# Performance work log

Measured on AMD Instinct MI355X. Metric: run time of the kernel, lower is better.

Reference implementation:

```python
import jax, jax.numpy as jnp
import numpy as np

B, H, W, C, NH, WS, SS = 32, 56, 56, 192, 6, 7, 3
L = H * W
N = WS * WS
HD = C // NH
EPS = 1e-3  # keras LayerNormalization default epsilon


def _rel_index(ws):
    coords = np.stack(np.meshgrid(np.arange(ws), np.arange(ws), indexing='ij')).reshape(2, -1)
    rel = (coords[:, :, None] - coords[:, None, :]).transpose(1, 2, 0)
    rel[..., 0] += ws - 1
    rel[..., 1] += ws - 1
    rel[..., 0] *= 2 * ws - 1
    return rel.sum(-1)  # (N, N) int


def _attn_mask(h, w, ws, ss):
    img = np.zeros((h, w), np.float32)
    cnt = 0
    for hs in (slice(0, -ws), slice(-ws, -ss), slice(-ss, None)):
        for wsl in (slice(0, -ws), slice(-ws, -ss), slice(-ss, None)):
            img[hs, wsl] = cnt
            cnt += 1
    mw = img.reshape(h // ws, ws, w // ws, ws).transpose(0, 2, 1, 3).reshape(-1, ws * ws)
    diff = mw[:, None, :] - mw[:, :, None]  # expand_dims(mw,1) - expand_dims(mw,2)
    return np.where(diff != 0, -100.0, 0.0).astype(np.float32)  # (nW, N, N)


REL_IDX = _rel_index(WS)
ATTN_MASK = _attn_mask(H, W, WS, SS)


def _ln(x, g, b):
    m = x.mean(-1, keepdims=True)
    v = x.var(-1, keepdims=True)
    return (x - m) / jnp.sqrt(v + EPS) * g + b


def setup_inputs() -> dict:
    key = jax.random.key(0)
    ks = jax.random.split(key, 8)
    s = 0.02
    return {
        'x': jax.random.normal(ks[0], (B, L, C), jnp.float32),
        'gamma1': jnp.ones((C,), jnp.float32),
        'beta1': jnp.zeros((C,), jnp.float32),
        'qkv_w': jax.random.normal(ks[1], (C, 3 * C), jnp.float32) * s,
        'qkv_b': jnp.zeros((3 * C,), jnp.float32),
        'proj_w': jax.random.normal(ks[2], (C, C), jnp.float32) * s,
        'proj_b': jnp.zeros((C,), jnp.float32),
        'rel_bias_table': jax.random.normal(ks[3], ((2 * WS - 1) ** 2, NH), jnp.float32) * s,
        'gamma2': jnp.ones((C,), jnp.float32),
        'beta2': jnp.zeros((C,), jnp.float32),
        'fc1_w': jax.random.normal(ks[4], (C, 4 * C), jnp.float32) * s,
        'fc1_b': jnp.zeros((4 * C,), jnp.float32),
        'fc2_w': jax.random.normal(ks[5], (4 * C, C), jnp.float32) * s,
        'fc2_b': jnp.zeros((C,), jnp.float32),
    }


def reference(x, gamma1, beta1, qkv_w, qkv_b, proj_w, proj_b, rel_bias_table,
              gamma2, beta2, fc1_w, fc1_b, fc2_w, fc2_b):
    scale = HD ** -0.5
    shortcut = x
    # norm1 + cyclic shift + window partition
    xn = _ln(x, gamma1, beta1).reshape(B, H, W, C)
    xn = jnp.roll(xn, (-SS, -SS), axis=(1, 2))
    xw = xn.reshape(B, H // WS, WS, W // WS, WS, C).transpose(0, 1, 3, 2, 4, 5).reshape(-1, N, C)
    # window attention
    qkv = (xw @ qkv_w + qkv_b).reshape(-1, N, 3, NH, HD).transpose(2, 0, 3, 1, 4)
    q, k, v = qkv[0] * scale, qkv[1], qkv[2]  # (B*nW, NH, N, HD)
    attn = jnp.einsum('whnd,whmd->whnm', q, k)
    bias = rel_bias_table[REL_IDX.reshape(-1)].reshape(N, N, NH).transpose(2, 0, 1)
    attn = attn + bias[None]
    nW = ATTN_MASK.shape[0]
    attn = attn.reshape(B, nW, NH, N, N) + jnp.asarray(ATTN_MASK)[None, :, None]
    attn = jax.nn.softmax(attn.reshape(-1, NH, N, N), axis=-1)
    out = jnp.einsum('whnm,whmd->whnd', attn, v).transpose(0, 2, 1, 3).reshape(-1, N, C)
    out = out @ proj_w + proj_b
    # window reverse + reverse shift
    xr = out.reshape(B, H // WS, W // WS, WS, WS, C).transpose(0, 1, 3, 2, 4, 5).reshape(B, H, W, C)
    xr = jnp.roll(xr, (SS, SS), axis=(1, 2)).reshape(B, L, C)
    x = shortcut + xr
    # MLP block
    y = _ln(x, gamma2, beta2)
    y = jax.nn.gelu(y @ fc1_w + fc1_b, approximate=False) @ fc2_w + fc2_b
    return x + y
```

## Files before the change

### kernel.cpp

```cpp
#include <hip/hip_runtime.h>
#include <math.h>

namespace {
constexpr int kBatch = 32, kH = 56, kW = 56, kC = 192, kNH = 6, kWS = 7, kSS = 3;
constexpr int kL   = kH * kW;
constexpr int kN   = kWS * kWS;
constexpr int kTok = kBatch * kL;
constexpr int kNWin = kTok / kN;
constexpr float kEps   = 1e-3f;
constexpr float kScale = 0.17677669529663687f;
}

typedef unsigned short u16;
typedef __attribute__((ext_vector_type(8))) short short8;
typedef __attribute__((ext_vector_type(4))) float f32x4;

__device__ __forceinline__ float bf2f(u16 u) {
    return __uint_as_float(((unsigned int)u) << 16);
}
__device__ __forceinline__ u16 f2bf(float f) {
    unsigned int x = __float_as_uint(f);
    return (u16)((x + 0x7FFFu + ((x >> 16) & 1u)) >> 16);
}
__device__ __forceinline__ float gelu_f(float x) {
    float z = 0.7978845608028654f * x * (1.0f + 0.044715f * x * x);
    float t = 1.0f - 2.0f / (1.0f + __expf(2.0f * z));
    return 0.5f * x * (1.0f + t);
}

__global__ __launch_bounds__(256) void ln_kernel(
    const float* __restrict__ x, const float* __restrict__ gamma,
    const float* __restrict__ beta, u16* __restrict__ out, int do_shift)
{
    const int wave = threadIdx.x >> 6;
    const int lane = threadIdx.x & 63;
    const int tok = (blockIdx.x << 2) + wave;
    const float* xp = x + (size_t)tok * kC;
    float v0 = xp[lane], v1 = xp[lane + 64], v2 = xp[lane + 128];
    float s  = v0 + v1 + v2;
    float sq = v0 * v0 + v1 * v1 + v2 * v2;
    #pragma unroll
    for (int off = 32; off > 0; off >>= 1) {
        s  += __shfl_down(s, off, 64);
        sq += __shfl_down(sq, off, 64);
    }
    s  = __shfl(s, 0, 64);
    sq = __shfl(sq, 0, 64);
    const float mean = s * (1.0f / kC);
    const float var  = sq * (1.0f / kC) - mean * mean;
    const float inv  = rsqrtf(var + kEps);
    size_t orow;
    if (do_shift) {
        const int b = tok / kL, hw = tok % kL;
        const int h = hw / kW, w = hw % kW;
        const int hs = (h + kH - kSS) % kH;
        const int ws = (w + kW - kSS) % kW;
        const int wh = hs / kWS, ii = hs % kWS;
        const int ww = ws / kWS, jj = ws % kWS;
        orow = (size_t)(b * 64 + wh * 8 + ww) * kN + (ii * kWS + jj);
    } else {
        orow = tok;
    }
    u16* op = out + orow * kC;
    op[lane]       = f2bf((v0 - mean) * inv * gamma[lane]       + beta[lane]);
    op[lane + 64]  = f2bf((v1 - mean) * inv * gamma[lane + 64]  + beta[lane + 64]);
    op[lane + 128] = f2bf((v2 - mean) * inv * gamma[lane + 128] + beta[lane + 128]);
}

__global__ __launch_bounds__(256) void wprep_qkv(
    const float* __restrict__ w, u16* __restrict__ wt)
{
    const int idx = blockIdx.x * 256 + threadIdx.x;
    if (idx >= 576 * 192) return;
    const int n = idx / 192, k = idx - n * 192;
    float v = w[(size_t)k * 576 + n];
    if (n < 192) v *= kScale;
    wt[idx] = f2bf(v);
}

__global__ __launch_bounds__(256) void wprep_rest(
    const float* __restrict__ pw, const float* __restrict__ f1w,
    const float* __restrict__ f2w, u16* __restrict__ proj_t,
    u16* __restrict__ f1_t, u16* __restrict__ f2_t, int* __restrict__ rowmap)
{
    int idx = blockIdx.x * 256 + threadIdx.x;
    if (idx < 36864) {
        const int n = idx / 192, k = idx - n * 192;
        proj_t[idx] = f2bf(pw[(size_t)k * 192 + n]);
        return;
    }
    idx -= 36864;
    if (idx < 147456) {
        const int n = idx / 192, k = idx - n * 192;
        f1_t[idx] = f2bf(f1w[(size_t)k * 768 + n]);
        return;
    }
    idx -= 147456;
    if (idx < 147456) {
        const int n = idx / 768, k = idx - n * 768;
        f2_t[idx] = f2bf(f2w[(size_t)k * 192 + n]);
        return;
    }
    idx -= 147456;
    if (idx < kTok) {
        const int win = idx / kN, n = idx - win * kN;
        const int b = win >> 6, wi = win & 63;
        const int wh = wi >> 3, ww = wi & 7;
        const int i1 = n / kWS, j1 = n - i1 * kWS;
        const int h = (wh * kWS + i1 + kSS) % kH;
        const int w = (ww * kWS + j1 + kSS) % kW;
        rowmap[idx] = b * kL + h * kW + w;
    }
}

__global__ __launch_bounds__(256) void prep_bm(
    const float* __restrict__ btab, const float* __restrict__ qkv_b,
    float* __restrict__ T, float* __restrict__ qkv_bs)
{
    const int idx = blockIdx.x * 256 + threadIdx.x;
    if (idx < 576) qkv_bs[idx] = (idx < 192) ? qkv_b[idx] * kScale : qkv_b[idx];
    if (idx >= 4 * 6 * 49 * 49) return;
    const int m = idx % 49, n = (idx / 49) % 49;
    const int head = (idx / 2401) % 6, cls = idx / (2401 * 6);
    const int i1 = n / 7, j1 = n % 7, i2 = m / 7, j2 = m % 7;
    float v = btab[((i1 - i2 + 6) * 13 + (j1 - j2 + 6)) * kNH + head];
    const int whE = cls >> 1, wwE = cls & 1;
    const int r1 = (whE ? (i1 < 4 ? 1 : 2) : 0) * 3 + (wwE ? (j1 < 4 ? 1 : 2) : 0);
    const int r2 = (whE ? (i2 < 4 ? 1 : 2) : 0) * 3 + (wwE ? (j2 < 4 ? 1 : 2) : 0);
    if (r1 != r2) v -= 100.f;
    T[idx] = v;
}

template <int MODE, int K, int NJ>
__global__ __launch_bounds__(256) void gemm_mfma(
    const u16* __restrict__ A, const u16* __restrict__ Bt, int ldb,
    const float* __restrict__ bias, const float* __restrict__ aux,
    void* __restrict__ outv, u16* __restrict__ vt = nullptr)
{
    constexpr int Nn = NJ * 192;
    constexpr int Kp = K + 8;
    __shared__ u16 As[64 * Kp];
    const int tid  = threadIdx.x;
    const int wave = tid >> 6, lane = tid & 63;
    const int quad = lane >> 4, l15 = lane & 15;
    const int m0 = blockIdx.x * 64;

    {
        const u16* src = A + (size_t)m0 * K;
        #pragma unroll
        for (int i = tid; i < 64 * K / 8; i += 256) {
            const int e = i * 8;
            const int r = e / K, c = e - r * K;
            *(short8*)&As[r * Kp + c] = *(const short8*)(src + e);
        }
    }
    __syncthreads();

    #pragma unroll
    for (int j = 0; j < NJ; ++j) {
        const int nb0 = j * 192 + wave * 48;
        const u16* Bbase = Bt + (size_t)(nb0 + l15) * ldb + quad * 8;
        f32x4 acc[4][3] = {};
        #pragma unroll
        for (int ks = 0; ks < K / 32; ++ks) {
            short8 a[4], b[3];
            #pragma unroll
            for (int i = 0; i < 4; ++i)
                a[i] = *(const short8*)&As[(i * 16 + l15) * Kp + ks * 32 + quad * 8];
            #pragma unroll
            for (int t = 0; t < 3; ++t)
                b[t] = *(const short8*)(Bbase + (size_t)t * 16 * ldb + ks * 32);
            #pragma unroll
            for (int i = 0; i < 4; ++i)
                #pragma unroll
                for (int t = 0; t < 3; ++t)
                    acc[i][t] = __builtin_amdgcn_mfma_f32_16x16x32_bf16(
                        a[i], b[t], acc[i][t], 0, 0, 0);
        }
        float bcol[3] = {0.f, 0.f, 0.f};
        {
            #pragma unroll
            for (int t = 0; t < 3; ++t) bcol[t] = bias[nb0 + t * 16 + l15];
        }
        #pragma unroll
        for (int i = 0; i < 4; ++i) {
            #pragma unroll
            for (int reg = 0; reg < 4; ++reg) {
                const int r = m0 + i * 16 + quad * 4 + reg;
                if (MODE == 5 && j == 2) {
                    const int win = r / kN, n = r - win * kN;
                    #pragma unroll
                    for (int t = 0; t < 3; ++t) {
                        const int d = nb0 - 384 + t * 16 + l15;
                        const size_t off =
                            ((size_t)win * 192 + d) * 64 + n;
                        vt[off] = f2bf(acc[i][t][reg] + bcol[t]);
                    }
                } else {
                    #pragma unroll
                    for (int t = 0; t < 3; ++t) {
                        const int c = nb0 + t * 16 + l15;
                        float v = acc[i][t][reg] + bcol[t];
                        ((u16*)outv)[(size_t)r * Nn + c] = f2bf(v);
                    }
                }
            }
        }
    }
}

__global__ __launch_bounds__(256) void proj_mlp_fused(
    const u16* __restrict__ A,
    const u16* __restrict__ proj_t, const float* __restrict__ proj_b,
    const float* __restrict__ x,
    const int* __restrict__ rowmap,
    const float* __restrict__ gamma, const float* __restrict__ beta,
    const u16* __restrict__ f1_t, const float* __restrict__ fc1_b,
    const u16* __restrict__ f2_t, const float* __restrict__ fc2_b,
    float* __restrict__ out)
{
    constexpr int Kp = 200;
    constexpr int Hp = 200;
    __shared__ u16 As[64 * Kp];
    __shared__ u16 Hs[64 * Hp];
    __shared__ int rowdest[64];
    const int tid  = threadIdx.x;
    const int wave = tid >> 6, lane = tid & 63;
    const int quad = lane >> 4, l15 = lane & 15;
    const int m0 = blockIdx.x * 64;
    float* Hsf = (float*)Hs;

    {
        const u16* src = A + (size_t)m0 * 192;
        #pragma unroll
        for (int i = tid; i < 64 * 192 / 8; i += 256) {
            const int e = i * 8;
            const int r = e / 192, c = e - r * 192;
            *(short8*)&As[r * Kp + c] = *(const short8*)(src + e);
        }
        if (tid < 64) rowdest[tid] = rowmap[m0 + tid];
    }
    __syncthreads();

    float x1[4][3][4];
    #pragma unroll
    for (int i = 0; i < 4; ++i) {
        #pragma unroll
        for (int reg = 0; reg < 4; ++reg) {
            const float* xr = x + (size_t)rowdest[i * 16 + quad * 4 + reg] * kC
                              + wave * 48 + l15;
            #pragma unroll
            for (int t = 0; t < 3; ++t) x1[i][t][reg] = xr[t * 16];
        }
    }

    f32x4 acc[4][3] = {};
    {
        const u16* Bbase = proj_t + (size_t)(wave * 48 + l15) * 192 + quad * 8;
        #pragma unroll
        for (int ks = 0; ks < 6; ++ks) {
            short8 a[4], b[3];
            #pragma unroll
            for (int i = 0; i < 4; ++i)
                a[i] = *(const short8*)&As[(i * 16 + l15) * Kp + ks * 32 + quad * 8];
            #pragma unroll
            for (int t = 0; t < 3; ++t)
                b[t] = *(const short8*)(Bbase + (size_t)t * 16 * 192 + ks * 32);
            #pragma unroll
            for (int i = 0; i < 4; ++i)
                #pragma unroll
                for (int t = 0; t < 3; ++t)
                    acc[i][t] = __builtin_amdgcn_mfma_f32_16x16x32_bf16(
                        a[i], b[t], acc[i][t], 0, 0, 0);
        }
    }
    {
        float bcol[3];
        #pragma unroll
        for (int t = 0; t < 3; ++t) bcol[t] = proj_b[wave * 48 + t * 16 + l15];
        #pragma unroll
        for (int i = 0; i < 4; ++i)
            #pragma unroll
            for (int t = 0; t < 3; ++t)
                #pragma unroll
                for (int reg = 0; reg < 4; ++reg)
                    x1[i][t][reg] += acc[i][t][reg] + bcol[t];
    }

    #pragma unroll
    for (int i = 0; i < 4; ++i) {
        #pragma unroll
        for (int reg = 0; reg < 4; ++reg) {
            float s  = x1[i][0][reg] + x1[i][1][reg] + x1[i][2][reg];
            float sq = x1[i][0][reg] * x1[i][0][reg]
                     + x1[i][1][reg] * x1[i][1][reg]
                     + x1[i][2][reg] * x1[i][2][reg];
            #pragma unroll
            for (int off = 1; off < 16; off <<= 1) {
                s  += __shfl_xor(s, off, 64);
                sq += __shfl_xor(sq, off, 64);
            }
            if (l15 == 0) {
                const int r = i * 16 + quad * 4 + reg;
                Hsf[r * 8 + wave * 2]     = s;
                Hsf[r * 8 + wave * 2 + 1] = sq;
            }
        }
    }
    __syncthreads();
    if (tid < 64) {
        const float s  = Hsf[tid * 8] + Hsf[tid * 8 + 2] + Hsf[tid * 8 + 4] + Hsf[tid * 8 + 6];
        const float sq = Hsf[tid * 8 + 1] + Hsf[tid * 8 + 3] + Hsf[tid * 8 + 5] + Hsf[tid * 8 + 7];
        const float mean = s * (1.0f / kC);
        const float inv  = rsqrtf(sq * (1.0f / kC) - mean * mean + kEps);
        Hsf[512 + tid * 2]     = mean;
        Hsf[512 + tid * 2 + 1] = inv;
    }
    __syncthreads();
    {
        float gv[3], bv[3];
        #pragma unroll
        for (int t = 0; t < 3; ++t) {
            gv[t] = gamma[wave * 48 + t * 16 + l15];
            bv[t] = beta[wave * 48 + t * 16 + l15];
        }
        #pragma unroll
        for (int i = 0; i < 4; ++i) {
            #pragma unroll
            for (int reg = 0; reg < 4; ++reg) {
                const int r = i * 16 + quad * 4 + reg;
                const float mean = Hsf[512 + r * 2];
                const float inv  = Hsf[513 + r * 2];
                #pragma unroll
                for (int t = 0; t < 3; ++t)
                    As[r * Kp + wave * 48 + t * 16 + l15] =
                        f2bf((x1[i][t][reg] - mean) * inv * gv[t] + bv[t]);
            }
        }
    }
    __syncthreads();

    f32x4 acc2[4][3] = {};
    for (int c = 0; c < 4; ++c) {
        f32x4 acc1[4][3] = {};
        {
            const u16* B1 = f1_t + (size_t)(c * 192 + wave * 48 + l15) * 192 + quad * 8;
            #pragma unroll
            for (int ks = 0; ks < 6; ++ks) {
                short8 a[4], b[3];
                #pragma unroll
                for (int i = 0; i < 4; ++i)
                    a[i] = *(const short8*)&As[(i * 16 + l15) * Kp + ks * 32 + quad * 8];
                #pragma unroll
                for (int t = 0; t < 3; ++t)
                    b[t] = *(const short8*)(B1 + (size_t)t * 16 * 192 + ks * 32);
                #pragma unroll
                for (int i = 0; i < 4; ++i)
                    #pragma unroll
                    for (int t = 0; t < 3; ++t)
                        acc1[i][t] = __builtin_amdgcn_mfma_f32_16x16x32_bf16(
                            a[i], b[t], acc1[i][t], 0, 0, 0);
            }
        }
        __syncthreads();
        #pragma unroll
        for (int t = 0; t < 3; ++t) {
            const int cc = wave * 48 + t * 16 + l15;
            const float bb = fc1_b[c * 192 + cc];
            #pragma unroll
            for (int i = 0; i < 4; ++i) {
                #pragma unroll
                for (int reg = 0; reg < 4; ++reg) {
                    const int r = i * 16 + quad * 4 + reg;
                    Hs[r * Hp + cc] = f2bf(gelu_f(acc1[i][t][reg] + bb));
                }
            }
        }
        __syncthreads();
        {
            const u16* B2 = f2_t + (size_t)(wave * 48 + l15) * 768 + c * 192 + quad * 8;
            #pragma unroll
            for (int ks = 0; ks < 6; ++ks) {
                short8 a[4], b[3];
                #pragma unroll
                for (int i = 0; i < 4; ++i)
                    a[i] = *(const short8*)&Hs[(i * 16 + l15) * Hp + ks * 32 + quad * 8];
                #pragma unroll
                for (int t = 0; t < 3; ++t)
                    b[t] = *(const short8*)(B2 + (size_t)t * 16 * 768 + ks * 32);
                #pragma unroll
                for (int i = 0; i < 4; ++i)
                    #pragma unroll
                    for (int t = 0; t < 3; ++t)
                        acc2[i][t] = __builtin_amdgcn_mfma_f32_16x16x32_bf16(
                            a[i], b[t], acc2[i][t], 0, 0, 0);
            }
        }
    }
    #pragma unroll
    for (int t = 0; t < 3; ++t) {
        const int cc = wave * 48 + t * 16 + l15;
        const float bb = fc2_b[cc];
        #pragma unroll
        for (int i = 0; i < 4; ++i) {
            #pragma unroll
            for (int reg = 0; reg < 4; ++reg) {
                const int dr = rowdest[i * 16 + quad * 4 + reg];
                out[(size_t)dr * kC + cc] = x1[i][t][reg] + acc2[i][t][reg] + bb;
            }
        }
    }
}

__global__ __launch_bounds__(256) void attn_mfma(
    const u16* __restrict__ qkv, const u16* __restrict__ vt,
    const float* __restrict__ T, u16* __restrict__ out)
{
    __shared__ u16 Ps[4][64][72];
    const int tid = threadIdx.x;
    const int wave = tid >> 6, lane = tid & 63;
    const int quad = lane >> 4, l15 = lane & 15;
    const int pair = blockIdx.x * 4 + wave;
    const int win = pair / 6, head = pair - win * 6;
    const int wi = win & 63;
    const int cls = (((wi >> 3) == 7) ? 2 : 0) + (((wi & 7) == 7) ? 1 : 0);
    const float* Tb = T + (size_t)(cls * 6 + head) * 49 * 49;

    const u16* base = qkv + (size_t)win * 49 * 576 + head * 32 + quad * 8;
    short8 zz = {};
    short8 qa[4], kb[4];
    #pragma unroll
    for (int i = 0; i < 4; ++i) {
        const int n = i * 16 + l15;
        qa[i] = (n < 49) ? *(const short8*)(base + (size_t)n * 576) : zz;
        kb[i] = (n < 49) ? *(const short8*)(base + (size_t)n * 576 + 192) : zz;
    }
    f32x4 acc[4][4];
    #pragma unroll
    for (int i = 0; i < 4; ++i) {
        #pragma unroll
        for (int reg = 0; reg < 4; ++reg) {
            const int n = i * 16 + quad * 4 + reg;
            const bool nv = (n < 49);
            const float* Trow = Tb + (nv ? n : 0) * 49;
            #pragma unroll
            for (int j = 0; j < 3; ++j)
                acc[i][j][reg] = nv ? Trow[j * 16 + l15] : 0.f;
            acc[i][3][reg] = (nv && l15 == 0) ? Trow[48] : -30000.f;
        }
    }
    #pragma unroll
    for (int i = 0; i < 4; ++i)
        #pragma unroll
        for (int j = 0; j < 4; ++j)
            acc[i][j] = __builtin_amdgcn_mfma_f32_16x16x32_bf16(
                qa[i], kb[j], acc[i][j], 0, 0, 0);
    float rowinv[4][4];
    #pragma unroll
    for (int i = 0; i < 4; ++i) {
        #pragma unroll
        for (int reg = 0; reg < 4; ++reg) {
            const int n = i * 16 + quad * 4 + reg;
            float e0 = __expf(acc[i][0][reg]), e1 = __expf(acc[i][1][reg]);
            float e2 = __expf(acc[i][2][reg]), e3 = __expf(acc[i][3][reg]);
            float sum = e0 + e1 + e2 + e3;
            #pragma unroll
            for (int off = 1; off < 16; off <<= 1)
                sum += __shfl_xor(sum, off, 64);
            rowinv[i][reg] = 1.0f / sum;
            Ps[wave][n][0 * 16 + l15] = f2bf(e0);
            Ps[wave][n][1 * 16 + l15] = f2bf(e1);
            Ps[wave][n][2 * 16 + l15] = f2bf(e2);
            Ps[wave][n][3 * 16 + l15] = f2bf(e3);
        }
    }
    const u16* vb_base = vt + ((size_t)pair * 32 + l15) * 64 + quad * 8;
    f32x4 o[4][2] = {};
    #pragma unroll
    for (int ks = 0; ks < 2; ++ks) {
        short8 pa[4], vb[2];
        #pragma unroll
        for (int i = 0; i < 4; ++i)
            pa[i] = *(const short8*)&Ps[wave][i * 16 + l15][ks * 32 + quad * 8];
        #pragma unroll
        for (int t = 0; t < 2; ++t)
            vb[t] = *(const short8*)(vb_base + (size_t)t * 16 * 64 + ks * 32);
        #pragma unroll
        for (int i = 0; i < 4; ++i)
            #pragma unroll
            for (int t = 0; t < 2; ++t)
                o[i][t] = __builtin_amdgcn_mfma_f32_16x16x32_bf16(
                    pa[i], vb[t], o[i][t], 0, 0, 0);
    }
    u16* obase = out + (size_t)win * 49 * 192 + head * 32;
    #pragma unroll
    for (int i = 0; i < 4; ++i) {
        #pragma unroll
        for (int reg = 0; reg < 4; ++reg) {
            const int n = i * 16 + quad * 4 + reg;
            if (n < 49) {
                const float inv = rowinv[i][reg];
                obase[(size_t)n * 192 + l15]      = f2bf(o[i][0][reg] * inv);
                obase[(size_t)n * 192 + 16 + l15] = f2bf(o[i][1][reg] * inv);
            }
        }
    }
}

extern "C" void kernel_launch(void* const* d_in, const int* in_sizes, int n_in,
                              void* d_out, int out_size, void* d_ws, size_t ws_size,
                              hipStream_t stream)
{
    const float* x      = (const float*)d_in[0];
    const float* gamma1 = (const float*)d_in[1];
    const float* beta1  = (const float*)d_in[2];
    const float* qkv_w  = (const float*)d_in[3];
    const float* qkv_b  = (const float*)d_in[4];
    const float* proj_w = (const float*)d_in[5];
    const float* proj_b = (const float*)d_in[6];
    const float* btab   = (const float*)d_in[7];
    const float* gamma2 = (const float*)d_in[8];
    const float* beta2  = (const float*)d_in[9];
    const float* fc1_w  = (const float*)d_in[10];
    const float* fc1_b  = (const float*)d_in[11];
    const float* fc2_w  = (const float*)d_in[12];
    const float* fc2_b  = (const float*)d_in[13];
    float* out = (float*)d_out;

    u16* buf_a = (u16*)d_ws;
    u16* buf_b = buf_a + (size_t)kTok * 192;
    u16* qkv_t = (u16*)d_out;
    float* bm_tab = (float*)d_out + 55296;
    float* qkv_bs = bm_tab + 57624;
    u16* vT = (u16*)d_out + 230400;
    u16* wt2   = (u16*)d_ws + (size_t)kTok * 768 - 331776;
    u16* proj_t = wt2;
    u16* f1_t   = wt2 + 36864;
    u16* f2_t   = f1_t + 147456;
    int* rowmap = (int*)buf_b;

    wprep_qkv<<<(110592 + 255) / 256, 256, 0, stream>>>(qkv_w, qkv_t);
    prep_bm<<<(57624 + 255) / 256, 256, 0, stream>>>(btab, qkv_b, bm_tab, qkv_bs);
    ln_kernel<<<kTok / 4, 256, 0, stream>>>(x, gamma1, beta1, buf_a, 1);
    gemm_mfma<5, 192, 3><<<kTok / 64, 256, 0, stream>>>(
        buf_a, qkv_t, 192, qkv_bs, nullptr, buf_b, vT);
    attn_mfma<<<(kNWin * kNH) / 4, 256, 0, stream>>>(buf_b, vT, bm_tab, buf_a);
    wprep_rest<<<(331776 + kTok + 255) / 256, 256, 0, stream>>>(
        proj_w, fc1_w, fc2_w, proj_t, f1_t, f2_t, rowmap);
    proj_mlp_fused<<<kTok / 64, 256, 0, stream>>>(
        buf_a, proj_t, proj_b, x, rowmap,
        gamma2, beta2, f1_t, fc1_b, f2_t, fc2_b, out);
}
```

Before: 498.1 us.

## Fuse LayerNorm with shifted-window gather into QKV GEMM and prefetch weight fragments

Folds the first LayerNorm and the cyclic-shift window gather into the QKV GEMM kernel: each block gathers its 64 source rows from x, normalizes them in registers and writes bf16 directly to shared memory. This removes the intermediate bf16 activation buffer round-trip and one launch. The rowmap table is replaced by on-the-fly index computation, and the proj/fc1/fc2 MFMA loops now double-buffer B fragments from global memory, one k-step ahead. The prefetching raises register pressure, which could reduce occupancy.

Measured after the change: 484.1 us. 1.03x faster.

```diff
diff --git a/kernel.cpp b/kernel.cpp
--- a/kernel.cpp
+++ b/kernel.cpp
@@ -28,43 +28,14 @@
     return 0.5f * x * (1.0f + t);
 }
 
-__global__ __launch_bounds__(256) void ln_kernel(
-    const float* __restrict__ x, const float* __restrict__ gamma,
-    const float* __restrict__ beta, u16* __restrict__ out, int do_shift)
-{
-    const int wave = threadIdx.x >> 6;
-    const int lane = threadIdx.x & 63;
-    const int tok = (blockIdx.x << 2) + wave;
-    const float* xp = x + (size_t)tok * kC;
-    float v0 = xp[lane], v1 = xp[lane + 64], v2 = xp[lane + 128];
-    float s  = v0 + v1 + v2;
-    float sq = v0 * v0 + v1 * v1 + v2 * v2;
-    #pragma unroll
-    for (int off = 32; off > 0; off >>= 1) {
-        s  += __shfl_down(s, off, 64);
-        sq += __shfl_down(sq, off, 64);
-    }
-    s  = __shfl(s, 0, 64);
-    sq = __shfl(sq, 0, 64);
-    const float mean = s * (1.0f / kC);
-    const float var  = sq * (1.0f / kC) - mean * mean;
-    const float inv  = rsqrtf(var + kEps);
-    size_t orow;
-    if (do_shift) {
-        const int b = tok / kL, hw = tok % kL;
-        const int h = hw / kW, w = hw % kW;
-        const int hs = (h + kH - kSS) % kH;
-        const int ws = (w + kW - kSS) % kW;
-        const int wh = hs / kWS, ii = hs % kWS;
-        const int ww = ws / kWS, jj = ws % kWS;
-        orow = (size_t)(b * 64 + wh * 8 + ww) * kN + (ii * kWS + jj);
-    } else {
-        orow = tok;
-    }
-    u16* op = out + orow * kC;
-    op[lane]       = f2bf((v0 - mean) * inv * gamma[lane]       + beta[lane]);
-    op[lane + 64]  = f2bf((v1 - mean) * inv * gamma[lane + 64]  + beta[lane + 64]);
-    op[lane + 128] = f2bf((v2 - mean) * inv * gamma[lane + 128] + beta[lane + 128]);
+__device__ __forceinline__ int win_row_to_tok(int idx) {
+    const int win = idx / kN, n = idx - win * kN;
+    const int b = win >> 6, wi = win & 63;
+    const int wh = wi >> 3, ww = wi & 7;
+    const int i1 = n / kWS, j1 = n - i1 * kWS;
+    const int h = (wh * kWS + i1 + kSS) % kH;
+    const int w = (ww * kWS + j1 + kSS) % kW;
+    return b * kL + h * kW + w;
 }
 
 __global__ __launch_bounds__(256) void wprep_qkv(
@@ -81,7 +52,7 @@
 __global__ __launch_bounds__(256) void wprep_rest(
     const float* __restrict__ pw, const float* __restrict__ f1w,
     const float* __restrict__ f2w, u16* __restrict__ proj_t,
-    u16* __restrict__ f1_t, u16* __restrict__ f2_t, int* __restrict__ rowmap)
+    u16* __restrict__ f1_t, u16* __restrict__ f2_t)
 {
     int idx = blockIdx.x * 256 + threadIdx.x;
     if (idx < 36864) {
@@ -99,17 +70,6 @@
     if (idx < 147456) {
         const int n = idx / 768, k = idx - n * 768;
         f2_t[idx] = f2bf(f2w[(size_t)k * 192 + n]);
-        return;
-    }
-    idx -= 147456;
-    if (idx < kTok) {
-        const int win = idx / kN, n = idx - win * kN;
-        const int b = win >> 6, wi = win & 63;
-        const int wh = wi >> 3, ww = wi & 7;
-        const int i1 = n / kWS, j1 = n - i1 * kWS;
-        const int h = (wh * kWS + i1 + kSS) % kH;
-        const int w = (ww * kWS + j1 + kSS) % kW;
-        rowmap[idx] = b * kL + h * kW + w;
     }
 }
 
@@ -131,45 +91,74 @@
     T[idx] = v;
 }
 
-template <int MODE, int K, int NJ>
-__global__ __launch_bounds__(256) void gemm_mfma(
-    const u16* __restrict__ A, const u16* __restrict__ Bt, int ldb,
-    const float* __restrict__ bias, const float* __restrict__ aux,
-    void* __restrict__ outv, u16* __restrict__ vt = nullptr)
-{
-    constexpr int Nn = NJ * 192;
-    constexpr int Kp = K + 8;
+__global__ __launch_bounds__(256) void ln_qkv(
+    const float* __restrict__ x, const float* __restrict__ gamma,
+    const float* __restrict__ beta,
+    const u16* __restrict__ qkv_t, const float* __restrict__ qkv_bs,
+    u16* __restrict__ qk_out, u16* __restrict__ vt)
+{
+    constexpr int Kp = 200;
     __shared__ u16 As[64 * Kp];
+    __shared__ int rowsrc[64];
     const int tid  = threadIdx.x;
     const int wave = tid >> 6, lane = tid & 63;
     const int quad = lane >> 4, l15 = lane & 15;
     const int m0 = blockIdx.x * 64;
 
+    if (tid < 64) rowsrc[tid] = win_row_to_tok(m0 + tid);
+    __syncthreads();
+
     {
-        const u16* src = A + (size_t)m0 * K;
-        #pragma unroll
-        for (int i = tid; i < 64 * K / 8; i += 256) {
-            const int e = i * 8;
-            const int r = e / K, c = e - r * K;
-            *(short8*)&As[r * Kp + c] = *(const short8*)(src + e);
+        float gv[12], bv[12];
+        #pragma unroll
+        for (int j = 0; j < 12; ++j) {
+            gv[j] = gamma[l15 * 12 + j];
+            bv[j] = beta[l15 * 12 + j];
+        }
+        #pragma unroll
+        for (int it = 0; it < 4; ++it) {
+            const int r = it * 16 + wave * 4 + quad;
+            const float* xp = x + (size_t)rowsrc[r] * kC + l15 * 12;
+            float4 u0 = *(const float4*)(xp);
+            float4 u1 = *(const float4*)(xp + 4);
+            float4 u2 = *(const float4*)(xp + 8);
+            float v[12] = {u0.x, u0.y, u0.z, u0.w, u1.x, u1.y, u1.z, u1.w,
+                           u2.x, u2.y, u2.z, u2.w};
+            float s = 0.f, sq = 0.f;
+            #pragma unroll
+            for (int j = 0; j < 12; ++j) { s += v[j]; sq += v[j] * v[j]; }
+            #pragma unroll
+            for (int off = 1; off < 16; off <<= 1) {
+                s  += __shfl_xor(s, off, 64);
+                sq += __shfl_xor(sq, off, 64);
+            }
+            const float mean = s * (1.0f / kC);
+            const float inv  = rsqrtf(sq * (1.0f / kC) - mean * mean + kEps);
+            unsigned* ap = (unsigned*)&As[r * Kp + l15 * 12];
+            #pragma unroll
+            for (int j = 0; j < 6; ++j) {
+                float a0 = (v[2 * j]     - mean) * inv * gv[2 * j]     + bv[2 * j];
+                float a1 = (v[2 * j + 1] - mean) * inv * gv[2 * j + 1] + bv[2 * j + 1];
+                ap[j] = (unsigned)f2bf(a0) | ((unsigned)f2bf(a1) << 16);
+            }
         }
     }
     __syncthreads();
 
     #pragma unroll
-    for (int j = 0; j < NJ; ++j) {
+    for (int j = 0; j < 3; ++j) {
         const int nb0 = j * 192 + wave * 48;
-        const u16* Bbase = Bt + (size_t)(nb0 + l15) * ldb + quad * 8;
+        const u16* Bbase = qkv_t + (size_t)(nb0 + l15) * 192 + quad * 8;
         f32x4 acc[4][3] = {};
         #pragma unroll
-        for (int ks = 0; ks < K / 32; ++ks) {
+        for (int ks = 0; ks < 6; ++ks) {
             short8 a[4], b[3];
             #pragma unroll
             for (int i = 0; i < 4; ++i)
                 a[i] = *(const short8*)&As[(i * 16 + l15) * Kp + ks * 32 + quad * 8];
             #pragma unroll
             for (int t = 0; t < 3; ++t)
-                b[t] = *(const short8*)(Bbase + (size_t)t * 16 * ldb + ks * 32);
+                b[t] = *(const short8*)(Bbase + (size_t)t * 16 * 192 + ks * 32);
             #pragma unroll
             for (int i = 0; i < 4; ++i)
                 #pragma unroll
@@ -177,17 +166,15 @@
                     acc[i][t] = __builtin_amdgcn_mfma_f32_16x16x32_bf16(
                         a[i], b[t], acc[i][t], 0, 0, 0);
         }
-        float bcol[3] = {0.f, 0.f, 0.f};
-        {
-            #pragma unroll
-            for (int t = 0; t < 3; ++t) bcol[t] = bias[nb0 + t * 16 + l15];
-        }
+        float bcol[3];
+        #pragma unroll
+        for (int t = 0; t < 3; ++t) bcol[t] = qkv_bs[nb0 + t * 16 + l15];
         #pragma unroll
         for (int i = 0; i < 4; ++i) {
             #pragma unroll
             for (int reg = 0; reg < 4; ++reg) {
                 const int r = m0 + i * 16 + quad * 4 + reg;
-                if (MODE == 5 && j == 2) {
+                if (j == 2) {
                     const int win = r / kN, n = r - win * kN;
                     #pragma unroll
                     for (int t = 0; t < 3; ++t) {
@@ -200,8 +187,8 @@
                     #pragma unroll
                     for (int t = 0; t < 3; ++t) {
                         const int c = nb0 + t * 16 + l15;
-                        float v = acc[i][t][reg] + bcol[t];
-                        ((u16*)outv)[(size_t)r * Nn + c] = f2bf(v);
+                        qk_out[(size_t)r * 576 + c] =
+                            f2bf(acc[i][t][reg] + bcol[t]);
                     }
                 }
             }
@@ -213,7 +200,6 @@
     const u16* __restrict__ A,
     const u16* __restrict__ proj_t, const float* __restrict__ proj_b,
     const float* __restrict__ x,
-    const int* __restrict__ rowmap,
     const float* __restrict__ gamma, const float* __restrict__ beta,
     const u16* __restrict__ f1_t, const float* __restrict__ fc1_b,
     const u16* __restrict__ f2_t, const float* __restrict__ fc2_b,
@@ -238,7 +224,7 @@
             const int r = e / 192, c = e - r * 192;
             *(short8*)&As[r * Kp + c] = *(const short8*)(src + e);
         }
-        if (tid < 64) rowdest[tid] = rowmap[m0 + tid];
+        if (tid < 64) rowdest[tid] = win_row_to_tok(m0 + tid);
     }
     __syncthreads();
 
@@ -257,21 +243,32 @@
     f32x4 acc[4][3] = {};
     {
         const u16* Bbase = proj_t + (size_t)(wave * 48 + l15) * 192 + quad * 8;
+        short8 bc[3], bn[3];
+        #pragma unroll
+        for (int t = 0; t < 3; ++t)
+            bc[t] = *(const short8*)(Bbase + (size_t)t * 16 * 192);
         #pragma unroll
         for (int ks = 0; ks < 6; ++ks) {
-            short8 a[4], b[3];
+            if (ks < 5) {
+                #pragma unroll
+                for (int t = 0; t < 3; ++t)
+                    bn[t] = *(const short8*)(Bbase + (size_t)t * 16 * 192 +
+                                             (ks + 1) * 32);
+            }
+            short8 a[4];
             #pragma unroll
             for (int i = 0; i < 4; ++i)
                 a[i] = *(const short8*)&As[(i * 16 + l15) * Kp + ks * 32 + quad * 8];
             #pragma unroll
-            for (int t = 0; t < 3; ++t)
-                b[t] = *(const short8*)(Bbase + (size_t)t * 16 * 192 + ks * 32);
-            #pragma unroll
             for (int i = 0; i < 4; ++i)
                 #pragma unroll
                 for (int t = 0; t < 3; ++t)
                     acc[i][t] = __builtin_amdgcn_mfma_f32_16x16x32_bf16(
-                        a[i], b[t], acc[i][t], 0, 0, 0);
+                        a[i], bc[t], acc[i][t], 0, 0, 0);
+            if (ks < 5) {
+                #pragma unroll
+                for (int t = 0; t < 3; ++t) bc[t] = bn[t];
+            }
         }
     }
     {
@@ -345,21 +342,32 @@
         f32x4 acc1[4][3] = {};
         {
             const u16* B1 = f1_t + (size_t)(c * 192 + wave * 48 + l15) * 192 + quad * 8;
+            short8 bc[3], bn[3];
+            #pragma unroll
+            for (int t = 0; t < 3; ++t)
+                bc[t] = *(const short8*)(B1 + (size_t)t * 16 * 192);
             #pragma unroll
             for (int ks = 0; ks < 6; ++ks) {
-                short8 a[4], b[3];
+                if (ks < 5) {
+                    #pragma unroll
+                    for (int t = 0; t < 3; ++t)
+                        bn[t] = *(const short8*)(B1 + (size_t)t * 16 * 192 +
+                                                 (ks + 1) * 32);
+                }
+                short8 a[4];
                 #pragma unroll
                 for (int i = 0; i < 4; ++i)
                     a[i] = *(const short8*)&As[(i * 16 + l15) * Kp + ks * 32 + quad * 8];
                 #pragma unroll
-                for (int t = 0; t < 3; ++t)
-                    b[t] = *(const short8*)(B1 + (size_t)t * 16 * 192 + ks * 32);
-                #pragma unroll
                 for (int i = 0; i < 4; ++i)
                     #pragma unroll
                     for (int t = 0; t < 3; ++t)
                         acc1[i][t] = __builtin_amdgcn_mfma_f32_16x16x32_bf16(
-                            a[i], b[t], acc1[i][t], 0, 0, 0);
+                            a[i], bc[t], acc1[i][t], 0, 0, 0);
+                if (ks < 5) {
+                    #pragma unroll
+                    for (int t = 0; t < 3; ++t) bc[t] = bn[t];
+                }
             }
         }
         __syncthreads();
@@ -379,21 +387,32 @@
         __syncthreads();
         {
             const u16* B2 = f2_t + (size_t)(wave * 48 + l15) * 768 + c * 192 + quad * 8;
+            short8 bc[3], bn[3];
+            #pragma unroll
+            for (int t = 0; t < 3; ++t)
+                bc[t] = *(const short8*)(B2 + (size_t)t * 16 * 768);
             #pragma unroll
             for (int ks = 0; ks < 6; ++ks) {
-                short8 a[4], b[3];
+                if (ks < 5) {
+                    #pragma unroll
+                    for (int t = 0; t < 3; ++t)
+                        bn[t] = *(const short8*)(B2 + (size_t)t * 16 * 768 +
+                                                 (ks + 1) * 32);
+                }
+                short8 a[4];
                 #pragma unroll
                 for (int i = 0; i < 4; ++i)
                     a[i] = *(const short8*)&Hs[(i * 16 + l15) * Hp + ks * 32 + quad * 8];
                 #pragma unroll
-                for (int t = 0; t < 3; ++t)
-                    b[t] = *(const short8*)(B2 + (size_t)t * 16 * 768 + ks * 32);
-                #pragma unroll
                 for (int i = 0; i < 4; ++i)
                     #pragma unroll
                     for (int t = 0; t < 3; ++t)
                         acc2[i][t] = __builtin_amdgcn_mfma_f32_16x16x32_bf16(
-                            a[i], b[t], acc2[i][t], 0, 0, 0);
+                            a[i], bc[t], acc2[i][t], 0, 0, 0);
+                if (ks < 5) {
+                    #pragma unroll
+                    for (int t = 0; t < 3; ++t) bc[t] = bn[t];
+                }
             }
         }
     }
@@ -537,17 +556,15 @@
     u16* proj_t = wt2;
     u16* f1_t   = wt2 + 36864;
     u16* f2_t   = f1_t + 147456;
-    int* rowmap = (int*)buf_b;
 
     wprep_qkv<<<(110592 + 255) / 256, 256, 0, stream>>>(qkv_w, qkv_t);
     prep_bm<<<(57624 + 255) / 256, 256, 0, stream>>>(btab, qkv_b, bm_tab, qkv_bs);
-    ln_kernel<<<kTok / 4, 256, 0, stream>>>(x, gamma1, beta1, buf_a, 1);
-    gemm_mfma<5, 192, 3><<<kTok / 64, 256, 0, stream>>>(
-        buf_a, qkv_t, 192, qkv_bs, nullptr, buf_b, vT);
+    ln_qkv<<<kTok / 64, 256, 0, stream>>>(
+        x, gamma1, beta1, qkv_t, qkv_bs, buf_b, vT);
     attn_mfma<<<(kNWin * kNH) / 4, 256, 0, stream>>>(buf_b, vT, bm_tab, buf_a);
-    wprep_rest<<<(331776 + kTok + 255) / 256, 256, 0, stream>>>(
-        proj_w, fc1_w, fc2_w, proj_t, f1_t, f2_t, rowmap);
+    wprep_rest<<<(331776 + 255) / 256, 256, 0, stream>>>(
+        proj_w, fc1_w, fc2_w, proj_t, f1_t, f2_t);
     proj_mlp_fused<<<kTok / 64, 256, 0, stream>>>(
-        buf_a, proj_t, proj_b, x, rowmap,
+        buf_a, proj_t, proj_b, x,
         gamma2, beta2, f1_t, fc1_b, f2_t, fc2_b, out);
 }
```
